# Optimization experiments

Measured on AMD Instinct MI355X. Metric: run time of the kernel, lower is better.

Reference implementation:

```python
import jax, jax.numpy as jnp
import numpy as np

PROP_TIME = 3
# (top,bottom),(left,right) zero-pad widths for the 8 neighbor shifts,
# matching torch ZeroPad2d((left,right,top,bottom)) in the original module.
PADS = [((0, 2), (0, 2)), ((0, 2), (1, 1)), ((0, 2), (2, 0)),
        ((1, 1), (0, 2)),                   ((1, 1), (2, 0)),
        ((2, 0), (0, 2)), ((2, 0), (1, 1)), ((2, 0), (2, 0))]


def _pad8(x, axis):
    """Pad last two dims 8 ways, stack the copies on `axis`."""
    lead = [(0, 0)] * (x.ndim - 2)
    return jnp.stack([jnp.pad(x, lead + [tb, lr]) for (tb, lr) in PADS], axis=axis)


def _affinity_norm(g):
    # g: [N, 8, H, W] -> gate_wb [N, 8, H+2, W+2], gate_sum [N, H, W]
    gw = jnp.stack([jnp.pad(g[:, k], [(0, 0), PADS[k][0], PADS[k][1]])
                    for k in range(8)], axis=1)
    abs_w = jnp.sum(jnp.abs(gw), axis=1, keepdims=True)
    gw = gw / abs_w
    gsum = jnp.sum(gw, axis=1)[:, 1:-1, 1:-1]
    return gw, gsum


def _propagate_once(gw, gsum, blur):
    # gw: [N,8,H+2,W+2], gsum: [N,H,W], blur: [N,B,H,W]
    nb = _pad8(blur, axis=1)                                # [N,8,B,H+2,W+2]
    ws = jnp.sum(gw[:, :, None] * nb, axis=1)[:, :, 1:-1, 1:-1]  # [N,B,H,W]
    return (1.0 - gsum[:, None]) * blur + ws


def _forward(guidance, blur, prop_time):
    # guidance: [24, X, Y, Z], blur: [B, X, Y, Z]
    gwx, gsx = _affinity_norm(jnp.transpose(guidance[0:8],   (3, 0, 1, 2)))  # [Z,8,X,Y]
    gwy, gsy = _affinity_norm(jnp.transpose(guidance[8:16],  (2, 0, 1, 3)))  # [Y,8,X,Z]
    gwz, gsz = _affinity_norm(jnp.transpose(guidance[16:24], (1, 0, 2, 3)))  # [X,8,Y,Z]
    r = blur
    for _ in range(prop_time):
        r = jnp.transpose(_propagate_once(gwx, gsx, jnp.transpose(r, (3, 0, 1, 2))), (1, 2, 3, 0))
        r = jnp.transpose(_propagate_once(gwy, gsy, jnp.transpose(r, (2, 0, 1, 3))), (1, 2, 0, 3))
        r = jnp.transpose(_propagate_once(gwz, gsz, jnp.transpose(r, (1, 0, 2, 3))), (1, 0, 2, 3))
    return r


def setup_inputs() -> dict:
    key = jax.random.key(0)
    k1, k2 = jax.random.split(key)
    guidance = jax.random.normal(k1, (24, 256, 256, 32), dtype=jnp.float32)
    blur = jax.random.normal(k2, (1, 256, 256, 32), dtype=jnp.float32)
    return {"guidance": guidance, "blur": blur}


def reference(guidance, blur):
    return _forward(guidance, blur, PROP_TIME)
```

## Files before the change

### kernel.cpp

```cpp
#include <hip/hip_runtime.h>
#include <hip/hip_fp16.h>


constexpr int NV = 256 * 256 * 32;
constexpr int YZ = 256 * 32;
constexpr int NG = NV / 4;
constexpr int GEND = 24 * NV;

struct alignas(16) H8 { __half2 h[4]; };

__device__ __forceinline__ int iclamp(int v, int lo, int hi) {
    return min(max(v, lo), hi);
}

__device__ __forceinline__ void unpack8(const H8& r, float* w) {
    float2 f;
    f = __half22float2(r.h[0]); w[0] = f.x; w[1] = f.y;
    f = __half22float2(r.h[1]); w[2] = f.x; w[3] = f.y;
    f = __half22float2(r.h[2]); w[4] = f.x; w[5] = f.y;
    f = __half22float2(r.h[3]); w[6] = f.x; w[7] = f.y;
}

template <int DIR>
__device__ __forceinline__ void wgroup_t(int f0, const float* __restrict__ g,
                                         H8* __restrict__ wt) {
    constexpr int d1[8] = {1, 1, 1, 0, 0, -1, -1, -1};
    constexpr int d2[8] = {1, 0, -1, 1, -1, 1, 0, -1};
    const int z = f0 & 31, y = (f0 >> 5) & 255, x = f0 >> 13;
    const int gb0 = DIR * 8 * NV;

    float G[8][4];

    if (DIR == 0) {
#pragma unroll
        for (int k = 0; k < 8; ++k) {
            const int a = x + d1[k], b = y + d2[k];
            const bool valid = ((unsigned)a < 256u) & ((unsigned)b < 256u);
            const int ofs = f0 + d1[k] * YZ + d2[k] * 32;
            float4 gv = *(const float4*)(g + iclamp(gb0 + k * NV + ofs, 0, GEND - 4));
            if (!valid) { gv.x = 0.f; gv.y = 0.f; gv.z = 0.f; gv.w = 0.f; }
            G[k][0] = gv.x; G[k][1] = gv.y; G[k][2] = gv.z; G[k][3] = gv.w;
        }
    } else {
        const int s1 = (DIR == 1) ? YZ : 32;
        const int c1 = (DIR == 1) ? x : y;
        const bool zlo = (z > 0), zhi = (z < 28);
#pragma unroll
        for (int k = 0; k < 8; ++k) {
            const bool vrow = (unsigned)(c1 + d1[k]) < 256u;
            const int gb = gb0 + k * NV + f0 + d1[k] * s1;
            float4 gv = *(const float4*)(g + iclamp(gb, 0, GEND - 4));
            if (!vrow) { gv.x = 0.f; gv.y = 0.f; gv.z = 0.f; gv.w = 0.f; }
            if (d2[k] == 1) {
                float ge = g[iclamp(gb + 4, 0, GEND - 1)];
                ge = (vrow && zhi) ? ge : 0.f;
                G[k][0] = gv.y; G[k][1] = gv.z; G[k][2] = gv.w; G[k][3] = ge;
            } else if (d2[k] == -1) {
                float ge = g[iclamp(gb - 1, 0, GEND - 1)];
                ge = (vrow && zlo) ? ge : 0.f;
                G[k][0] = ge; G[k][1] = gv.x; G[k][2] = gv.y; G[k][3] = gv.z;
            } else {
                G[k][0] = gv.x; G[k][1] = gv.y; G[k][2] = gv.z; G[k][3] = gv.w;
            }
        }
    }

#pragma unroll
    for (int i = 0; i < 4; ++i) {
        float asum = 0.f;
#pragma unroll
        for (int k = 0; k < 8; ++k) asum += fabsf(G[k][i]);
        const float winv = __builtin_amdgcn_rcpf(asum);
        H8 rec;
#pragma unroll
        for (int p = 0; p < 4; ++p)
            rec.h[p] = __floats2half2_rn(G[2 * p][i] * winv, G[2 * p + 1][i] * winv);
        wt[DIR * NV + f0 + i] = rec;
    }
}

__global__ __launch_bounds__(256) void make_w(const float* __restrict__ g,
                                              H8* __restrict__ wt) {
    const int b = blockIdx.x;
    const int dir = b >> 11;
    const int f0 = ((b & 2047) * 256 + threadIdx.x) << 2;
    if (dir == 0)      wgroup_t<0>(f0, g, wt);
    else if (dir == 1) wgroup_t<1>(f0, g, wt);
    else               wgroup_t<2>(f0, g, wt);
}

template <int DIR>
__global__ __launch_bounds__(256) void wstep(const H8* __restrict__ wt,
                                             const float* __restrict__ rin,
                                             float* __restrict__ rout) {
    constexpr int d1[8] = {1, 1, 1, 0, 0, -1, -1, -1};
    constexpr int d2[8] = {1, 0, -1, 1, -1, 1, 0, -1};
    const int t = blockIdx.x * 256 + threadIdx.x;
    const int f0 = t << 2;

    const H8* wp = wt + DIR * NV + f0;
    float w[4][8];
#pragma unroll
    for (int i = 0; i < 4; ++i) unpack8(wp[i], w[i]);

    float a[4];

    if (DIR == 0) {
        const float4 rc = *(const float4*)(rin + f0);
        const float rc4[4] = {rc.x, rc.y, rc.z, rc.w};
        a[0] = rc.x; a[1] = rc.y; a[2] = rc.z; a[3] = rc.w;
#pragma unroll
        for (int k = 0; k < 8; ++k) {
            const int ofs = f0 + d1[k] * YZ + d2[k] * 32;
            const float4 rv = *(const float4*)(rin + iclamp(ofs, 0, NV - 4));
            const float nb[4] = {rv.x, rv.y, rv.z, rv.w};
#pragma unroll
            for (int i = 0; i < 4; ++i)
                a[i] = fmaf(w[i][k], nb[i] - rc4[i], a[i]);
        }
    } else {
        constexpr int s1 = (DIR == 1) ? YZ : 32;
        float e[3][6];
#pragma unroll
        for (int j = 0; j < 3; ++j) {
            const int ro = f0 + (1 - j) * s1;
            const float4 rv = *(const float4*)(rin + iclamp(ro, 0, NV - 4));
            e[j][0] = rin[iclamp(ro - 1, 0, NV - 1)];
            e[j][1] = rv.x; e[j][2] = rv.y; e[j][3] = rv.z; e[j][4] = rv.w;
            e[j][5] = rin[iclamp(ro + 4, 0, NV - 1)];
        }
        const float rc4[4] = {e[1][1], e[1][2], e[1][3], e[1][4]};
        a[0] = rc4[0]; a[1] = rc4[1]; a[2] = rc4[2]; a[3] = rc4[3];
#pragma unroll
        for (int k = 0; k < 8; ++k) {
            const int j = 1 - d1[k];
#pragma unroll
            for (int i = 0; i < 4; ++i)
                a[i] = fmaf(w[i][k], e[j][1 + i + d2[k]] - rc4[i], a[i]);
        }
    }

    *(float4*)(rout + f0) = make_float4(a[0], a[1], a[2], a[3]);
}

template <int DIR>
__global__ __launch_bounds__(256) void prop_step(const float* __restrict__ g,
                                                 const float* __restrict__ rin,
                                                 float* __restrict__ rout) {
    constexpr int d1[8] = {1, 1, 1, 0, 0, -1, -1, -1};
    constexpr int d2[8] = {1, 0, -1, 1, -1, 1, 0, -1};
    const int t = blockIdx.x * 256 + threadIdx.x;
    const int f0 = t << 2;
    const int z = f0 & 31, y = (f0 >> 5) & 255, x = f0 >> 13;
    const int gb0 = DIR * 8 * NV;

    float as[4] = {0, 0, 0, 0}, ac[4] = {0, 0, 0, 0};
    float4 rc;

    if (DIR == 0) {
        rc = *(const float4*)(rin + f0);
#pragma unroll
        for (int k = 0; k < 8; ++k) {
            const int a = x + d1[k], b = y + d2[k];
            const bool valid = ((unsigned)a < 256u) & ((unsigned)b < 256u);
            const int ofs = f0 + d1[k] * YZ + d2[k] * 32;
            const float4 rv = *(const float4*)(rin + iclamp(ofs, 0, NV - 4));
            float4 gv = *(const float4*)(g + iclamp(gb0 + k * NV + ofs, 0, GEND - 4));
            if (!valid) { gv.x = 0.f; gv.y = 0.f; gv.z = 0.f; gv.w = 0.f; }
            as[0] += fabsf(gv.x); as[1] += fabsf(gv.y);
            as[2] += fabsf(gv.z); as[3] += fabsf(gv.w);
            ac[0] = fmaf(gv.x, rv.x - rc.x, ac[0]); ac[1] = fmaf(gv.y, rv.y - rc.y, ac[1]);
            ac[2] = fmaf(gv.z, rv.z - rc.z, ac[2]); ac[3] = fmaf(gv.w, rv.w - rc.w, ac[3]);
        }
    } else {
        const int s1 = (DIR == 1) ? YZ : 32;
        const int c1 = (DIR == 1) ? x : y;
        float4 rv[3]; float rl[3], rr[3];
#pragma unroll
        for (int j = 0; j < 3; ++j) {
            const int ro = f0 + (1 - j) * s1;
            rv[j] = *(const float4*)(rin + iclamp(ro, 0, NV - 4));
            rl[j] = rin[iclamp(ro - 1, 0, NV - 1)];
            rr[j] = rin[iclamp(ro + 4, 0, NV - 1)];
        }
        rc = rv[1];
        const bool zlo = (z > 0), zhi = (z < 28);
#pragma unroll
        for (int k = 0; k < 8; ++k) {
            const int j = 1 - d1[k];
            const bool vrow = (unsigned)(c1 + d1[k]) < 256u;
            const int gb = gb0 + k * NV + f0 + d1[k] * s1;
            float4 gv = *(const float4*)(g + iclamp(gb, 0, GEND - 4));
            if (!vrow) { gv.x = 0.f; gv.y = 0.f; gv.z = 0.f; gv.w = 0.f; }
            float4 gk, rk;
            if (d2[k] == 1) {
                float ge = g[iclamp(gb + 4, 0, GEND - 1)];
                ge = (vrow && zhi) ? ge : 0.f;
                gk = make_float4(gv.y, gv.z, gv.w, ge);
                rk = make_float4(rv[j].y, rv[j].z, rv[j].w, rr[j]);
            } else if (d2[k] == -1) {
                float ge = g[iclamp(gb - 1, 0, GEND - 1)];
                ge = (vrow && zlo) ? ge : 0.f;
                gk = make_float4(ge, gv.x, gv.y, gv.z);
                rk = make_float4(rl[j], rv[j].x, rv[j].y, rv[j].z);
            } else {
                gk = gv; rk = rv[j];
            }
            as[0] += fabsf(gk.x); as[1] += fabsf(gk.y);
            as[2] += fabsf(gk.z); as[3] += fabsf(gk.w);
            ac[0] = fmaf(gk.x, rk.x - rc.x, ac[0]); ac[1] = fmaf(gk.y, rk.y - rc.y, ac[1]);
            ac[2] = fmaf(gk.z, rk.z - rc.z, ac[2]); ac[3] = fmaf(gk.w, rk.w - rc.w, ac[3]);
        }
    }

    float4 o;
    o.x = rc.x + ac[0] * __builtin_amdgcn_rcpf(as[0]);
    o.y = rc.y + ac[1] * __builtin_amdgcn_rcpf(as[1]);
    o.z = rc.z + ac[2] * __builtin_amdgcn_rcpf(as[2]);
    o.w = rc.w + ac[3] * __builtin_amdgcn_rcpf(as[3]);
    *(float4*)(rout + f0) = o;
}

extern "C" void kernel_launch(void* const* d_in, const int* in_sizes, int n_in,
                              void* d_out, int out_size, void* d_ws, size_t ws_size,
                              hipStream_t stream) {
    const float* g    = (const float*)d_in[0];
    const float* blur = (const float*)d_in[1];
    float* out = (float*)d_out;

    const size_t WBYTES = (size_t)3 * NV * sizeof(H8);
    const size_t NEED   = WBYTES + (size_t)2 * NV * sizeof(float);

    if (ws_size >= NEED) {
        H8*    wt   = (H8*)d_ws;
        float* bufA = (float*)((char*)d_ws + WBYTES);
        float* bufB = bufA + NV;

        make_w<<<dim3(3 * NG / 256), dim3(256), 0, stream>>>(g, wt);

        const float* src = blur;
        for (int step = 0; step < 9; ++step) {
            float* dst = (step == 8) ? out : ((step & 1) ? bufB : bufA);
            switch (step % 3) {
                case 0: wstep<0><<<dim3(NG / 256), dim3(256), 0, stream>>>(wt, src, dst); break;
                case 1: wstep<1><<<dim3(NG / 256), dim3(256), 0, stream>>>(wt, src, dst); break;
                case 2: wstep<2><<<dim3(NG / 256), dim3(256), 0, stream>>>(wt, src, dst); break;
            }
            src = dst;
        }
    } else {
        float* ws = (float*)d_ws;
        const dim3 block(256), sgrid(NG / 256);
        const float* src = blur;
        for (int step = 0; step < 9; ++step) {
            float* dst = (step & 1) ? ws : out;
            switch (step % 3) {
                case 0: prop_step<0><<<sgrid, block, 0, stream>>>(g, src, dst); break;
                case 1: prop_step<1><<<sgrid, block, 0, stream>>>(g, src, dst); break;
                case 2: prop_step<2><<<sgrid, block, 0, stream>>>(g, src, dst); break;
            }
            src = dst;
        }
    }
}
```

Before: 389.3 us.

## Fuse the three directional propagation steps per iteration into one LDS-tiled kernel

Replaces the nine separate per-direction step launches with three launches of a fused kernel. Each block loads an x-y tile of the volume with a halo and a 16-wide z chunk plus a z halo into shared memory, then applies the x, y and z passes in turn, keeping intermediate results in LDS. This removes two global round trips of the field per iteration. In exchange it recomputes halo cells, leaves some threads idle (only 240 of 256 are active, fewer in later passes), uses more shared memory per block, and adds block-wide synchronisation.

```diff
diff --git a/kernel.cpp b/kernel.cpp
--- a/kernel.cpp
+++ b/kernel.cpp
@@ -7,10 +7,22 @@
 constexpr int NG = NV / 4;
 constexpr int GEND = 24 * NV;
 
+constexpr int TXB = 8, TYB = 16;
+constexpr int RXD = 12, RYD = 20;
+constexpr int NCOL = RXD * RYD;
+constexpr int ZSTR = 24;
+constexpr int LOFFG = 4;
+constexpr int ASZP = LOFFG + 240 * ZSTR + 12;
+constexpr int BSZP = LOFFG + 180 * ZSTR + 12;
+
 struct alignas(16) H8 { __half2 h[4]; };
 
 __device__ __forceinline__ int iclamp(int v, int lo, int hi) {
     return min(max(v, lo), hi);
+}
+
+__device__ __forceinline__ int cbase(int c) {
+    return LOFFG + c * ZSTR;
 }
 
 __device__ __forceinline__ void unpack8(const H8& r, float* w) {
@@ -89,14 +101,160 @@
     else               wgroup_t<2>(f0, g, wt);
 }
 
+__global__ __launch_bounds__(256, 4) void iter_fused(const H8* __restrict__ wt,
+                                                     const float* __restrict__ rin,
+                                                     float* __restrict__ rout) {
+    __shared__ __align__(16) float A[ASZP];
+    __shared__ __align__(16) float B[BSZP];
+    constexpr int d1c[8] = {1, 1, 1, 0, 0, -1, -1, -1};
+    constexpr int d2c[8] = {1, 0, -1, 1, -1, 1, 0, -1};
+
+    const int t = threadIdx.x;
+    const int chunk = blockIdx.x & 1;
+    const int tile  = blockIdx.x >> 1;
+    const int bx = tile & 31, by = tile >> 5;
+    const bool act = t < NCOL;
+    const int rx = t / RYD, ry = t - rx * RYD;
+    const int gx = bx * TXB - 2 + rx, gy = by * TYB - 2 + ry;
+    const int gxc = iclamp(gx, 0, 255), gyc = iclamp(gy, 0, 255);
+    const int z0 = chunk * 16;
+    const int slot_base = chunk ? 0 : 4;
+    const int gz_base   = chunk ? 12 : 0;
+
+    for (int i = t; i < ASZP; i += 256) A[i] = 0.f;
+    for (int i = t; i < BSZP; i += 256) B[i] = 0.f;
+    __syncthreads();
+
+    if (act) {
+        const float* p = rin + ((gxc << 8) + gyc) * 32 + gz_base;
+        const int ab = cbase(t) + slot_base;
+#pragma unroll
+        for (int j = 0; j < 5; ++j)
+            *(float4*)(A + ab + 4 * j) = *(const float4*)(p + 4 * j);
+    }
+    __syncthreads();
+
+    const bool in0 = act && rx >= 1 && rx <= 10 && ry >= 1 && ry <= 18;
+    const bool in1 = act && rx >= 2 && rx <= 9  && ry >= 1 && ry <= 18;
+    const bool in2 = act && rx >= 2 && rx <= 9  && ry >= 2 && ry <= 17;
+    const int wvox = ((gxc << 8) + gyc) * 32;
+
+    if (in0) {
+        int nbb[8];
+#pragma unroll
+        for (int k = 0; k < 8; ++k)
+            nbb[k] = cbase((rx + d1c[k]) * RYD + (ry + d2c[k]));
+        const int ab = cbase(t);
+        const int bb = cbase((rx - 1) * 18 + (ry - 1));
+        const H8* wp = wt + wvox;
+#pragma unroll
+        for (int j = 0; j < 6; ++j) {
+            const int zs = z0 - 4 + 4 * j;
+            H8 wr[4];
+#pragma unroll
+            for (int i = 0; i < 4; ++i) wr[i] = wp[iclamp(zs + i, 0, 31)];
+            const float4 vc = *(const float4*)(A + ab + 4 * j);
+            const float rc4[4] = {vc.x, vc.y, vc.z, vc.w};
+            float nb[8][4];
+#pragma unroll
+            for (int k = 0; k < 8; ++k) {
+                const float4 v = *(const float4*)(A + nbb[k] + 4 * j);
+                nb[k][0] = v.x; nb[k][1] = v.y; nb[k][2] = v.z; nb[k][3] = v.w;
+            }
+            float o[4];
+#pragma unroll
+            for (int i = 0; i < 4; ++i) {
+                float w[8]; unpack8(wr[i], w);
+                float a = rc4[i];
+#pragma unroll
+                for (int k = 0; k < 8; ++k) a = fmaf(w[k], nb[k][i] - rc4[i], a);
+                o[i] = a;
+            }
+            *(float4*)(B + bb + 4 * j) = make_float4(o[0], o[1], o[2], o[3]);
+        }
+    }
+    __syncthreads();
+
+    if (in1) {
+        const int rowb[3] = {cbase(rx * 18 + (ry - 1)),
+                             cbase((rx - 1) * 18 + (ry - 1)),
+                             cbase((rx - 2) * 18 + (ry - 1))};
+        const int ab = cbase(t);
+        const H8* wp = wt + NV + wvox;
+#pragma unroll
+        for (int j = 0; j < 6; ++j) {
+            const int zs = z0 - 4 + 4 * j;
+            H8 wr[4];
+#pragma unroll
+            for (int i = 0; i < 4; ++i) wr[i] = wp[iclamp(zs + i, 0, 31)];
+            float e[3][6];
+#pragma unroll
+            for (int jr = 0; jr < 3; ++jr) {
+                const int cofs = rowb[jr] + 4 * j;
+                const float4 v = *(const float4*)(B + cofs);
+                e[jr][0] = B[cofs - 1];
+                e[jr][1] = v.x; e[jr][2] = v.y; e[jr][3] = v.z; e[jr][4] = v.w;
+                e[jr][5] = B[cofs + 4];
+            }
+            float o[4];
+#pragma unroll
+            for (int i = 0; i < 4; ++i) {
+                float w[8]; unpack8(wr[i], w);
+                const float rc = e[1][1 + i];
+                float a = rc;
+#pragma unroll
+                for (int k = 0; k < 8; ++k)
+                    a = fmaf(w[k], e[1 - d1c[k]][1 + i + d2c[k]] - rc, a);
+                o[i] = a;
+            }
+            *(float4*)(A + ab + 4 * j) = make_float4(o[0], o[1], o[2], o[3]);
+        }
+    }
+    __syncthreads();
+
+    if (in2) {
+        const int rowb[3] = {cbase(rx * RYD + (ry + 1)),
+                             cbase(rx * RYD + ry),
+                             cbase(rx * RYD + (ry - 1))};
+        const H8* wp = wt + 2 * NV + wvox;
+        float* gq = rout + ((gx << 8) + gy) * 32 + z0;
+#pragma unroll
+        for (int j = 0; j < 4; ++j) {
+            const int zs = z0 + 4 * j;
+            H8 wr[4];
+#pragma unroll
+            for (int i = 0; i < 4; ++i) wr[i] = wp[zs + i];
+            float e[3][6];
+#pragma unroll
+            for (int jr = 0; jr < 3; ++jr) {
+                const int cofs = rowb[jr] + 4 + 4 * j;
+                const float4 v = *(const float4*)(A + cofs);
+                e[jr][0] = A[cofs - 1];
+                e[jr][1] = v.x; e[jr][2] = v.y; e[jr][3] = v.z; e[jr][4] = v.w;
+                e[jr][5] = A[cofs + 4];
+            }
+            float o[4];
+#pragma unroll
+            for (int i = 0; i < 4; ++i) {
+                float w[8]; unpack8(wr[i], w);
+                const float rc = e[1][1 + i];
+                float a = rc;
+#pragma unroll
+                for (int k = 0; k < 8; ++k)
+                    a = fmaf(w[k], e[1 - d1c[k]][1 + i + d2c[k]] - rc, a);
+                o[i] = a;
+            }
+            *(float4*)(gq + 4 * j) = make_float4(o[0], o[1], o[2], o[3]);
+        }
+    }
+}
+
 template <int DIR>
-__global__ __launch_bounds__(256) void wstep(const H8* __restrict__ wt,
-                                             const float* __restrict__ rin,
-                                             float* __restrict__ rout) {
+__device__ __forceinline__ void step_body(const H8* __restrict__ wt,
+                                          const float* __restrict__ rin,
+                                          float* __restrict__ rout, int f0) {
     constexpr int d1[8] = {1, 1, 1, 0, 0, -1, -1, -1};
     constexpr int d2[8] = {1, 0, -1, 1, -1, 1, 0, -1};
-    const int t = blockIdx.x * 256 + threadIdx.x;
-    const int f0 = t << 2;
 
     const H8* wp = wt + DIR * NV + f0;
     float w[4][8];
@@ -141,6 +299,14 @@
     }
 
     *(float4*)(rout + f0) = make_float4(a[0], a[1], a[2], a[3]);
+}
+
+template <int DIR>
+__global__ __launch_bounds__(256) void wstep(const H8* __restrict__ wt,
+                                             const float* __restrict__ rin,
+                                             float* __restrict__ rout) {
+    const int f0 = (blockIdx.x * 256 + threadIdx.x) << 2;
+    step_body<DIR>(wt, rin, rout, f0);
 }
 
 template <int DIR>
@@ -237,17 +403,9 @@
         float* bufB = bufA + NV;
 
         make_w<<<dim3(3 * NG / 256), dim3(256), 0, stream>>>(g, wt);
-
-        const float* src = blur;
-        for (int step = 0; step < 9; ++step) {
-            float* dst = (step == 8) ? out : ((step & 1) ? bufB : bufA);
-            switch (step % 3) {
-                case 0: wstep<0><<<dim3(NG / 256), dim3(256), 0, stream>>>(wt, src, dst); break;
-                case 1: wstep<1><<<dim3(NG / 256), dim3(256), 0, stream>>>(wt, src, dst); break;
-                case 2: wstep<2><<<dim3(NG / 256), dim3(256), 0, stream>>>(wt, src, dst); break;
-            }
-            src = dst;
-        }
+        iter_fused<<<dim3(1024), dim3(256), 0, stream>>>(wt, blur, bufA);
+        iter_fused<<<dim3(1024), dim3(256), 0, stream>>>(wt, bufA, bufB);
+        iter_fused<<<dim3(1024), dim3(256), 0, stream>>>(wt, bufB, out);
     } else {
         float* ws = (float*)d_ws;
         const dim3 block(256), sgrid(NG / 256);
```

After: 414.1 us. +6.4%, slower.
